# Kernel optimization log

Measured on AMD Instinct MI355X. Metric: run time of the kernel, lower is better.

Reference implementation:

```python
import jax, jax.numpy as jnp
import numpy as np

# ---- module configuration (from init_kwargs) ----
NX, NV = 2048, 1024
LX = 1.0
VMAX = 6.0
DX = LX / NX
DV = 2.0 * VMAX / NV
XS = jnp.linspace(-LX / 2 + DX / 2, LX / 2 - DX / 2, NX)
VS = jnp.linspace(-VMAX + DV / 2, VMAX - DV / 2, NV)
AE, AI = 1.0, 1836.0
ZE, ZI = -1.0, 1.0
OMEGA_C_TAU = 1.0
NU_EE, NU_II = 1.0, 0.1
DT = 1e-3
T_LBO = 1.0  # LBO temperature, u = 0


def minmod(a, b):
    return jnp.where(a * b > 0, jnp.sign(a) * jnp.minimum(jnp.abs(a), jnp.abs(b)), 0.0)


def _sl(a, lo, hi, axis):
    return jax.lax.slice_in_dim(a, lo, hi, axis=axis)


def slope_limited_flux_divergence(f_pad, F, dx, axis):
    # f_pad has N+4 cells along `axis` (2 ghost cells per side). MUSCL + minmod.
    n = f_pad.shape[axis]
    d = _sl(f_pad, 1, n, axis) - _sl(f_pad, 0, n - 1, axis)          # n-1 diffs
    sigma = minmod(_sl(d, 0, n - 2, axis), _sl(d, 1, n - 1, axis))    # slopes for cells 1..n-2
    fc = _sl(f_pad, 1, n - 1, axis)                                   # cells 1..n-2
    m = n - 2
    fL = _sl(fc, 0, m - 1, axis) + 0.5 * _sl(sigma, 0, m - 1, axis)   # left interface states
    fR = _sl(fc, 1, m, axis) - 0.5 * _sl(sigma, 1, m, axis)           # right interface states
    flux = F(fL, fR)                                                  # N+1 interface fluxes
    k = flux.shape[axis]
    return (_sl(flux, 1, k, axis) - _sl(flux, 0, k - 1, axis)) / dx   # N cells


def pad_x_periodic(f):
    return jnp.concatenate([f[-2:, :], f, f[:2, :]], axis=0)


def pad_v_zero(f):
    z = jnp.zeros((f.shape[0], 2), f.dtype)
    return jnp.concatenate([z, f, z], axis=1)


def poisson_solve(rho_c):
    # dE/dx = rho_c, zero-mean E (periodic-compatible gauge)
    E = jnp.cumsum(rho_c) * DX
    return E - jnp.mean(E)


def species_rhs(f, E, A, Z):
    v = VS[None, :]
    Fx = lambda l, r: jnp.where(v > 0, l * v, r * v)                  # upwind in x
    vdfdx = slope_limited_flux_divergence(pad_x_periodic(f), Fx, DX, axis=0)
    Ec = (OMEGA_C_TAU * Z / A) * E[:, None]
    Fv = lambda l, r: jnp.where(Ec > 0, l * Ec, r * Ec)               # upwind in v
    Edfdv = slope_limited_flux_divergence(pad_v_zero(f), Fv, DV, axis=1)
    return -vdfdx - Edfdv


def vlasov_rhs(fe, fi):
    ne = jnp.sum(fe, axis=1) * DV
    ni = jnp.sum(fi, axis=1) * DV
    E = poisson_solve(ZE * ne + ZI * ni)
    return species_rhs(fe, E, AE, ZE), species_rhs(fi, E, AI, ZI)


def ssprk2(fe, fi, dt):
    re, ri = vlasov_rhs(fe, fi)
    fe1, fi1 = fe + dt * re, fi + dt * ri
    re1, ri1 = vlasov_rhs(fe1, fi1)
    return 0.5 * (fe + fe1 + dt * re1), 0.5 * (fi + fi1 + dt * ri1)


def lbo_diagonals(lam):
    # L f = lam * d/dv( v f + T df/dv ), central differences
    vm = jnp.roll(VS, 1)
    vp = jnp.roll(VS, -1)
    dl = lam * (T_LBO / DV**2 - vm / (2 * DV))
    du = lam * (T_LBO / DV**2 + vp / (2 * DV))
    d = lam * (-2.0 * T_LBO / DV**2) * jnp.ones(NV, XS.dtype)
    return dl.at[0].set(0.0), d, du.at[-1].set(0.0)


def nu_shape():
    midpt = LX / 3
    ef = LX / 6 / 10
    h0 = lambda x: 1 + jnp.exp(x / ef - midpt / ef)
    return 1.0 / (0.5 * (h0(XS) + h0(-XS)))  # [Nx]


def thomas(dl, d, du, b):
    # Thomas algorithm; dl[0]==0 and du[-1]==0 assumed.
    def fwd(carry, inp):
        cp, bp = carry
        dli, di, dui, bi = inp
        m = di - dli * cp
        cpi = dui / m
        bpi = (bi - dli * bp) / m
        return (cpi, bpi), (cpi, bpi)
    z = jnp.zeros((), b.dtype)
    _, (cp, bp) = jax.lax.scan(fwd, (z, z), (dl, d, du, b))
    def bwd(x_next, inp):
        cpi, bpi = inp
        x = bpi - cpi * x_next
        return x, x
    _, x = jax.lax.scan(bwd, z, (cp, bp), reverse=True)
    return x


def implicit_collide(f, lam, dt):
    dl, d, du = lbo_diagonals(lam)
    nu = nu_shape()
    def solve_row(nui, frow):
        return thomas(-dt * nui * dl, 1.0 - dt * nui * d, -dt * nui * du, frow)
    return jax.vmap(solve_row)(nu, f)


def setup_inputs() -> dict:
    key = jax.random.key(0)
    k1, k2 = jax.random.split(key)
    fe = jax.random.uniform(k1, (NX, NV), dtype=jnp.float32)
    fi = jax.random.uniform(k2, (NX, NV), dtype=jnp.float32)
    return {"fe": fe, "fi": fi}


def reference(fe, fi):
    fe1, fi1 = ssprk2(fe, fi, DT)
    fe2 = implicit_collide(fe1, NU_EE, DT)
    fi2 = implicit_collide(fi1, NU_II, DT)
    return jnp.stack([fe2, fi2])  # [2, Nx, Nv]
```

## Files before the change

kernel.cpp:

```cpp
#include <hip/hip_runtime.h>
#include <math.h>

#define NX 2048
#define NV 1024
static constexpr float DXf   = 1.0f / 2048.0f;
static constexpr float DVf   = 12.0f / 1024.0f;
static constexpr float DTf   = 0.001f;
static constexpr float INV_DX = 2048.0f;
static constexpr float INV_DV = 1024.0f / 12.0f;

__device__ __forceinline__ float minmod_f(float a, float b) {
    return (a * b > 0.0f) ? (a > 0.0f ? fminf(a, b) : fmaxf(a, b)) : 0.0f;
}

__device__ __forceinline__ float frcp(float x) {
    float r = __builtin_amdgcn_rcpf(x);
    return r * (2.0f - x * r);
}

__device__ __forceinline__ void rhs4(const float* __restrict__ g, int i, int j0, float Ec,
                                     float4& f0v, float4& rv) {
    const float* rowc = g + i * NV;
    const float* rm1  = g + (((i - 1) & (NX - 1)) * NV);
    const float* rm2  = g + (((i - 2) & (NX - 1)) * NV);
    const float* rp1  = g + (((i + 1) & (NX - 1)) * NV);
    const float* rp2  = g + (((i + 2) & (NX - 1)) * NV);

    float4 c   = *(const float4*)(rowc + j0);
    float4 xm1 = *(const float4*)(rm1 + j0);
    float4 xm2 = *(const float4*)(rm2 + j0);
    float4 xp1 = *(const float4*)(rp1 + j0);
    float4 xp2 = *(const float4*)(rp2 + j0);
    float4 lm = make_float4(0.f, 0.f, 0.f, 0.f);
    float4 rp = make_float4(0.f, 0.f, 0.f, 0.f);
    if (j0 >= 4)      lm = *(const float4*)(rowc + j0 - 4);
    if (j0 <= NV - 8) rp = *(const float4*)(rowc + j0 + 4);

    float vals[8] = {lm.z, lm.w, c.x, c.y, c.z, c.w, rp.x, rp.y};
    const float* cc   = (const float*)&c;
    const float* am1  = (const float*)&xm1;
    const float* am2  = (const float*)&xm2;
    const float* ap1  = (const float*)&xp1;
    const float* ap2  = (const float*)&xp2;
    float* f0o = (float*)&f0v;
    float* ro  = (float*)&rv;

    #pragma unroll
    for (int k = 0; k < 4; ++k) {
        float f0  = cc[k];
        float fm1 = am1[k], fm2 = am2[k], fp1 = ap1[k], fp2 = ap2[k];

        float v = DVf * ((float)(j0 + k) + 0.5f) - 6.0f;
        float dm1 = fm1 - fm2, d0 = f0 - fm1, dp1 = fp1 - f0, dp2 = fp2 - fp1;
        float sm1 = minmod_f(dm1, d0);
        float s0  = minmod_f(d0, dp1);
        float sp1 = minmod_f(dp1, dp2);
        float PhiM, PhiP;
        if (v > 0.0f) {
            PhiM = (fm1 + 0.5f * sm1) * v;
            PhiP = (f0  + 0.5f * s0 ) * v;
        } else {
            PhiM = (f0  - 0.5f * s0 ) * v;
            PhiP = (fp1 - 0.5f * sp1) * v;
        }
        float vdfdx = (PhiP - PhiM) * INV_DX;

        float gm2 = vals[k], gm1 = vals[k + 1], gp1 = vals[k + 3], gp2 = vals[k + 4];
        float em1 = gm1 - gm2, e0 = f0 - gm1, ep1 = gp1 - f0, ep2 = gp2 - gp1;
        float tm1 = minmod_f(em1, e0);
        float t0  = minmod_f(e0, ep1);
        float tp1 = minmod_f(ep1, ep2);
        float GM, GP;
        if (Ec > 0.0f) {
            GM = (gm1 + 0.5f * tm1) * Ec;
            GP = (f0  + 0.5f * t0 ) * Ec;
        } else {
            GM = (f0  - 0.5f * t0 ) * Ec;
            GP = (gp1 - 0.5f * tp1) * Ec;
        }
        float Edfdv = (GP - GM) * INV_DV;

        f0o[k] = f0;
        ro[k]  = -vdfdx - Edfdv;
    }
}

__device__ __forceinline__ float block_sum256(float x, float* sred) {
    #pragma unroll
    for (int off = 32; off > 0; off >>= 1) x += __shfl_down(x, off, 64);
    int lane = threadIdx.x & 63, wave = threadIdx.x >> 6;
    if (lane == 0) sred[wave] = x;
    __syncthreads();
    float r = 0.0f;
    if (threadIdx.x == 0) r = sred[0] + sred[1] + sred[2] + sred[3];
    return r;
}

__global__ __launch_bounds__(256) void moments_kernel(const float* __restrict__ fe,
                                                      const float* __restrict__ fi,
                                                      float* __restrict__ se,
                                                      float* __restrict__ si) {
    int i = blockIdx.x;
    int t = threadIdx.x;
    float4 a4 = *(const float4*)(fe + (size_t)i * NV + 4 * t);
    float4 b4 = *(const float4*)(fi + (size_t)i * NV + 4 * t);
    float a = a4.x + a4.y + a4.z + a4.w;
    float b = b4.x + b4.y + b4.z + b4.w;
    __shared__ float r1[4], r2[4];
    #pragma unroll
    for (int off = 32; off > 0; off >>= 1) {
        a += __shfl_down(a, off, 64);
        b += __shfl_down(b, off, 64);
    }
    int lane = t & 63, wave = t >> 6;
    if (lane == 0) { r1[wave] = a; r2[wave] = b; }
    __syncthreads();
    if (t == 0) {
        se[i] = r1[0] + r1[1] + r1[2] + r1[3];
        si[i] = r2[0] + r2[1] + r2[2] + r2[3];
    }
}

__global__ __launch_bounds__(1024) void poisson_kernel(const float* __restrict__ se,
                                                       const float* __restrict__ si,
                                                       float* __restrict__ E) {
    __shared__ float p[1024];
    __shared__ float red[1024];
    int t = threadIdx.x;
    float r0 = DVf * (si[2 * t]     - se[2 * t]);
    float r1 = DVf * (si[2 * t + 1] - se[2 * t + 1]);
    p[t] = r0 + r1;
    __syncthreads();
    for (int off = 1; off < 1024; off <<= 1) {
        float v = p[t];
        float add = (t >= off) ? p[t - off] : 0.0f;
        __syncthreads();
        p[t] = v + add;
        __syncthreads();
    }
    float Pexcl = (t > 0) ? p[t - 1] : 0.0f;
    float S0 = Pexcl + r0;
    float S1 = p[t];
    red[t] = S0 + S1;
    __syncthreads();
    for (int off = 512; off > 0; off >>= 1) {
        if (t < off) red[t] += red[t + off];
        __syncthreads();
    }
    float meanS = red[0] * (1.0f / (float)NX);
    E[2 * t]     = DXf * (S0 - meanS);
    E[2 * t + 1] = DXf * (S1 - meanS);
}

__global__ __launch_bounds__(256) void stage1_kernel(const float* __restrict__ fe,
                                                     const float* __restrict__ fi,
                                                     const float* __restrict__ E,
                                                     float* __restrict__ fe1,
                                                     float* __restrict__ fi1,
                                                     float* __restrict__ se1,
                                                     float* __restrict__ si1) {
    int i  = blockIdx.x;
    int sp = blockIdx.y;
    const float* g = sp ? fi : fe;
    float* out = sp ? fi1 : fe1;
    float zoa = sp ? (1.0f / 1836.0f) : -1.0f;
    float Ec = zoa * E[i];
    int t = threadIdx.x;
    int j0 = 4 * t;

    float4 f0v, rv;
    rhs4(g, i, j0, Ec, f0v, rv);
    float4 o;
    o.x = f0v.x + DTf * rv.x;
    o.y = f0v.y + DTf * rv.y;
    o.z = f0v.z + DTf * rv.z;
    o.w = f0v.w + DTf * rv.w;
    *(float4*)(out + i * NV + j0) = o;

    __shared__ float sred[4];
    float s = block_sum256(o.x + o.y + o.z + o.w, sred);
    if (t == 0) { (sp ? si1 : se1)[i] = s; }
}

__global__ __launch_bounds__(256) void stage2_collide_kernel(const float* __restrict__ fe,
                                                             const float* __restrict__ fi,
                                                             const float* __restrict__ fe1,
                                                             const float* __restrict__ fi1,
                                                             const float* __restrict__ E,
                                                             float* __restrict__ out) {
    const float Tdv2   = 1.0f / (DVf * DVf);
    const float inv2dv = 0.5f / DVf;

    int i  = blockIdx.x;
    int sp = blockIdx.y;
    const float* h = sp ? fi : fe;
    const float* g = sp ? fi1 : fe1;
    float* orow = out + ((size_t)sp * NX + i) * NV;
    float zoa = sp ? (1.0f / 1836.0f) : -1.0f;
    float lam = sp ? 0.1f : 1.0f;
    float Ec = zoa * E[i];
    int t = threadIdx.x;
    int lane = t & 63;
    int wave = t >> 6;

    __shared__ float lds_f[NV + NV / 16];

    {
        int j0 = 4 * t;
        float4 f0v, rv;
        rhs4(g, i, j0, Ec, f0v, rv);
        float4 h4 = *(const float4*)(h + i * NV + j0);
        int a = j0 + (j0 >> 4);
        lds_f[a]     = 0.5f * h4.x + 0.5f * f0v.x + (0.5f * DTf) * rv.x;
        lds_f[a + 1] = 0.5f * h4.y + 0.5f * f0v.y + (0.5f * DTf) * rv.y;
        lds_f[a + 2] = 0.5f * h4.z + 0.5f * f0v.z + (0.5f * DTf) * rv.z;
        lds_f[a + 3] = 0.5f * h4.w + 0.5f * f0v.w + (0.5f * DTf) * rv.w;
    }
    __syncthreads();
    if (wave != 0) return;

    float xi = DXf * ((float)i + 0.5f) - 0.5f;
    float nu = 1.0f / (1.0f + 0.5f * (expf(60.0f * xi - 20.0f) + expf(-60.0f * xi - 20.0f)));
    float K = DTf * nu * lam;
    float b = 1.0f + 2.0f * K * Tdv2;

    float Dv[16], Av[16], Cv[16];
    int j0 = lane * 16;
    int base = 17 * lane;
    #pragma unroll
    for (int r = 0; r < 16; ++r) {
        int j = j0 + r;
        float d = lds_f[base + r];
        float a = (j == 0)      ? 0.0f : -K * (Tdv2 - (DVf * ((float)j - 0.5f) - 6.0f) * inv2dv);
        float c = (j == NV - 1) ? 0.0f : -K * (Tdv2 + (DVf * ((float)j + 1.5f) - 6.0f) * inv2dv);
        if (r == 0) {
            float e = frcp(b);
            Dv[0] = e * d;
            Av[0] = e * a;
            Cv[0] = e * c;
        } else {
            float e = frcp(b - a * Cv[r - 1]);
            Dv[r] = e * (d - a * Dv[r - 1]);
            Av[r] = -e * a * Av[r - 1];
            Cv[r] = e * c;
        }
    }
    #pragma unroll
    for (int r = 14; r >= 0; --r) {
        Dv[r] = Dv[r] - Cv[r] * Dv[r + 1];
        Av[r] = Av[r] - Cv[r] * Av[r + 1];
        Cv[r] = -Cv[r] * Cv[r + 1];
    }

    float la = Av[0],  ra = Cv[0],  d0 = Dv[0];
    float lb = Av[15], rb = Cv[15], d1 = Dv[15];

    #pragma unroll
    for (int s = 1; s < 64; s <<= 1) {
        float lb_m = __shfl_up(lb, s, 64);
        float rb_m = __shfl_up(rb, s, 64);
        float d1_m = __shfl_up(d1, s, 64);
        if (lane < s) { lb_m = 0.0f; rb_m = 0.0f; d1_m = 0.0f; }
        float la_p = __shfl_down(la, s, 64);
        float ra_p = __shfl_down(ra, s, 64);
        float d0_p = __shfl_down(d0, s, 64);
        if (lane + s > 63) { la_p = 0.0f; ra_p = 0.0f; d0_p = 0.0f; }

        float m00 = 1.0f - la * rb_m;
        float m01 = -ra * la_p;
        float m10 = -lb * rb_m;
        float m11 = 1.0f - rb * la_p;
        float idet = frcp(m00 * m11 - m01 * m10);

        float Lr0 = -la * lb_m, Lr1 = -lb * lb_m;
        float Rr0 = -ra * ra_p, Rr1 = -rb * ra_p;
        float e0 = d0 - la * d1_m - ra * d0_p;
        float e1 = d1 - lb * d1_m - rb * d0_p;

        la = idet * (m11 * Lr0 - m01 * Lr1);
        lb = idet * (m00 * Lr1 - m10 * Lr0);
        ra = idet * (m11 * Rr0 - m01 * Rr1);
        rb = idet * (m00 * Rr1 - m10 * Rr0);
        d0 = idet * (m11 * e0 - m01 * e1);
        d1 = idet * (m00 * e1 - m10 * e0);
    }
    float zl = __shfl_up(d1, 1, 64);
    if (lane == 0) zl = 0.0f;
    float yr = __shfl_down(d0, 1, 64);
    if (lane == 63) yr = 0.0f;

    float x[16];
    #pragma unroll
    for (int r = 0; r < 16; ++r) x[r] = Dv[r] - Av[r] * zl - Cv[r] * yr;
    #pragma unroll
    for (int q = 0; q < 4; ++q) {
        float4 o;
        o.x = x[4 * q];
        o.y = x[4 * q + 1];
        o.z = x[4 * q + 2];
        o.w = x[4 * q + 3];
        *(float4*)(orow + j0 + 4 * q) = o;
    }
}

extern "C" void kernel_launch(void* const* d_in, const int* in_sizes, int n_in,
                              void* d_out, int out_size, void* d_ws, size_t ws_size,
                              hipStream_t stream) {
    const float* fe = (const float*)d_in[0];
    const float* fi = (const float*)d_in[1];
    float* out = (float*)d_out;
    const size_t P = (size_t)NX * NV;

    float* fe1 = (float*)d_ws;
    float* fi1 = fe1 + P;
    float* se  = fi1 + P;
    float* si  = se + NX;
    float* E   = si + NX;
    float* se1 = E + NX;
    float* si1 = se1 + NX;
    float* E1  = si1 + NX;

    dim3 rgrid(NX, 2);

    moments_kernel<<<NX, 256, 0, stream>>>(fe, fi, se, si);
    poisson_kernel<<<1, 1024, 0, stream>>>(se, si, E);
    stage1_kernel<<<rgrid, 256, 0, stream>>>(fe, fi, E, fe1, fi1, se1, si1);
    poisson_kernel<<<1, 1024, 0, stream>>>(se1, si1, E1);
    stage2_collide_kernel<<<rgrid, 256, 0, stream>>>(fe, fi, fe1, fi1, E1, out);
}
```

Before: 116.1 us.

## Fuse Poisson solve into stage kernels via per-block prefix and weighted sum

Removes the two single-block Poisson kernel launches. Each stage block now computes its own E[i] directly from the row sums: a prefix sum up to i, minus the mean, where the mean comes from a weighted sum with weights (NX-k). This drops two serialized, low-occupancy launches and their scans. In exchange every one of the 4096 blocks per stage redundantly reads 16 KB of moment data and does a block reduction, with some change in float summation order.

```diff
diff --git a/kernel.cpp b/kernel.cpp
--- a/kernel.cpp
+++ b/kernel.cpp
@@ -85,15 +85,29 @@
     }
 }
 
-__device__ __forceinline__ float block_sum256(float x, float* sred) {
-    #pragma unroll
-    for (int off = 32; off > 0; off >>= 1) x += __shfl_down(x, off, 64);
-    int lane = threadIdx.x & 63, wave = threadIdx.x >> 6;
-    if (lane == 0) sred[wave] = x;
+__device__ __forceinline__ float compute_E(const float* __restrict__ se,
+                                           const float* __restrict__ si, int i) {
+    int t = threadIdx.x;
+    float pref = 0.0f, wtot = 0.0f;
+    #pragma unroll
+    for (int q = 0; q < NX / 256; ++q) {
+        int k = q * 256 + t;
+        float rho = DVf * (si[k] - se[k]);
+        if (k <= i) pref += rho;
+        wtot += rho * (float)(NX - k);
+    }
+    #pragma unroll
+    for (int off = 32; off > 0; off >>= 1) {
+        pref += __shfl_down(pref, off, 64);
+        wtot += __shfl_down(wtot, off, 64);
+    }
+    __shared__ float sp[4], sw[4];
+    int lane = t & 63, wave = t >> 6;
+    if (lane == 0) { sp[wave] = pref; sw[wave] = wtot; }
     __syncthreads();
-    float r = 0.0f;
-    if (threadIdx.x == 0) r = sred[0] + sred[1] + sred[2] + sred[3];
-    return r;
+    float P = sp[0] + sp[1] + sp[2] + sp[3];
+    float W = sw[0] + sw[1] + sw[2] + sw[3];
+    return DXf * (P - W * (1.0f / (float)NX));
 }
 
 __global__ __launch_bounds__(256) void moments_kernel(const float* __restrict__ fe,
@@ -121,40 +135,10 @@
     }
 }
 
-__global__ __launch_bounds__(1024) void poisson_kernel(const float* __restrict__ se,
-                                                       const float* __restrict__ si,
-                                                       float* __restrict__ E) {
-    __shared__ float p[1024];
-    __shared__ float red[1024];
-    int t = threadIdx.x;
-    float r0 = DVf * (si[2 * t]     - se[2 * t]);
-    float r1 = DVf * (si[2 * t + 1] - se[2 * t + 1]);
-    p[t] = r0 + r1;
-    __syncthreads();
-    for (int off = 1; off < 1024; off <<= 1) {
-        float v = p[t];
-        float add = (t >= off) ? p[t - off] : 0.0f;
-        __syncthreads();
-        p[t] = v + add;
-        __syncthreads();
-    }
-    float Pexcl = (t > 0) ? p[t - 1] : 0.0f;
-    float S0 = Pexcl + r0;
-    float S1 = p[t];
-    red[t] = S0 + S1;
-    __syncthreads();
-    for (int off = 512; off > 0; off >>= 1) {
-        if (t < off) red[t] += red[t + off];
-        __syncthreads();
-    }
-    float meanS = red[0] * (1.0f / (float)NX);
-    E[2 * t]     = DXf * (S0 - meanS);
-    E[2 * t + 1] = DXf * (S1 - meanS);
-}
-
 __global__ __launch_bounds__(256) void stage1_kernel(const float* __restrict__ fe,
                                                      const float* __restrict__ fi,
-                                                     const float* __restrict__ E,
+                                                     const float* __restrict__ se,
+                                                     const float* __restrict__ si,
                                                      float* __restrict__ fe1,
                                                      float* __restrict__ fi1,
                                                      float* __restrict__ se1,
@@ -164,7 +148,7 @@
     const float* g = sp ? fi : fe;
     float* out = sp ? fi1 : fe1;
     float zoa = sp ? (1.0f / 1836.0f) : -1.0f;
-    float Ec = zoa * E[i];
+    float Ec = zoa * compute_E(se, si, i);
     int t = threadIdx.x;
     int j0 = 4 * t;
 
@@ -177,16 +161,22 @@
     o.w = f0v.w + DTf * rv.w;
     *(float4*)(out + i * NV + j0) = o;
 
+    float x = o.x + o.y + o.z + o.w;
+    #pragma unroll
+    for (int off = 32; off > 0; off >>= 1) x += __shfl_down(x, off, 64);
     __shared__ float sred[4];
-    float s = block_sum256(o.x + o.y + o.z + o.w, sred);
-    if (t == 0) { (sp ? si1 : se1)[i] = s; }
+    int lane = t & 63, wave = t >> 6;
+    if (lane == 0) sred[wave] = x;
+    __syncthreads();
+    if (t == 0) { (sp ? si1 : se1)[i] = sred[0] + sred[1] + sred[2] + sred[3]; }
 }
 
 __global__ __launch_bounds__(256) void stage2_collide_kernel(const float* __restrict__ fe,
                                                              const float* __restrict__ fi,
                                                              const float* __restrict__ fe1,
                                                              const float* __restrict__ fi1,
-                                                             const float* __restrict__ E,
+                                                             const float* __restrict__ se1,
+                                                             const float* __restrict__ si1,
                                                              float* __restrict__ out) {
     const float Tdv2   = 1.0f / (DVf * DVf);
     const float inv2dv = 0.5f / DVf;
@@ -198,7 +188,7 @@
     float* orow = out + ((size_t)sp * NX + i) * NV;
     float zoa = sp ? (1.0f / 1836.0f) : -1.0f;
     float lam = sp ? 0.1f : 1.0f;
-    float Ec = zoa * E[i];
+    float Ec = zoa * compute_E(se1, si1, i);
     int t = threadIdx.x;
     int lane = t & 63;
     int wave = t >> 6;
@@ -315,16 +305,12 @@
     float* fi1 = fe1 + P;
     float* se  = fi1 + P;
     float* si  = se + NX;
-    float* E   = si + NX;
-    float* se1 = E + NX;
+    float* se1 = si + NX;
     float* si1 = se1 + NX;
-    float* E1  = si1 + NX;
 
     dim3 rgrid(NX, 2);
 
     moments_kernel<<<NX, 256, 0, stream>>>(fe, fi, se, si);
-    poisson_kernel<<<1, 1024, 0, stream>>>(se, si, E);
-    stage1_kernel<<<rgrid, 256, 0, stream>>>(fe, fi, E, fe1, fi1, se1, si1);
-    poisson_kernel<<<1, 1024, 0, stream>>>(se1, si1, E1);
-    stage2_collide_kernel<<<rgrid, 256, 0, stream>>>(fe, fi, fe1, fi1, E1, out);
-}
+    stage1_kernel<<<rgrid, 256, 0, stream>>>(fe, fi, se, si, fe1, fi1, se1, si1);
+    stage2_collide_kernel<<<rgrid, 256, 0, stream>>>(fe, fi, fe1, fi1, se1, si1, out);
+}
```

After: 112.9 us. 1.03x faster.
